# Kernel tuning notes

Measured on AMD Instinct MI355X. Metric: run time of the kernel, lower is better.

## Reference

```python
import jax, jax.numpy as jnp
import numpy as np

NUM_HEADS = 12


def setup_inputs() -> dict:
    key = jax.random.key(0)
    ks = jax.random.split(key, 5)
    B, S, D = 4, 2048, 768
    scale = 0.02
    return {
        "hidden_states": jax.random.normal(ks[0], (B, S, D), dtype=jnp.float32),
        "c_attn_w": jax.random.normal(ks[1], (D, 3 * D), dtype=jnp.float32) * scale,
        "c_attn_b": jax.random.normal(ks[2], (3 * D,), dtype=jnp.float32) * scale,
        "c_proj_w": jax.random.normal(ks[3], (D, D), dtype=jnp.float32) * scale,
        "c_proj_b": jax.random.normal(ks[4], (D,), dtype=jnp.float32) * scale,
    }


def reference(hidden_states, c_attn_w, c_attn_b, c_proj_w, c_proj_b):
    B, S, D = hidden_states.shape
    H = NUM_HEADS
    hd = D // H

    # fused QKV projection (HF Conv1D: x @ W + b, W is [in, out])
    qkv = hidden_states @ c_attn_w + c_attn_b  # [B, S, 3D]
    q, k, v = jnp.split(qkv, 3, axis=-1)

    def split_heads(t):
        return t.reshape(B, S, H, hd).transpose(0, 2, 1, 3)  # [B, H, S, hd]

    q, k, v = split_heads(q), split_heads(k), split_heads(v)

    # scaled dot-product scores (scale_attn_weights=True -> / sqrt(head_dim))
    scores = jnp.einsum("bhqd,bhkd->bhqk", q, k) / jnp.asarray(
        np.sqrt(hd), dtype=q.dtype
    )

    # causal mask: where(tril, scores, dtype_min) as in eager GPT2Attention
    causal = jnp.tril(jnp.ones((S, S), dtype=bool))
    mask_value = jnp.finfo(scores.dtype).min
    scores = jnp.where(causal[None, None, :, :], scores, mask_value)

    attn = jax.nn.softmax(scores, axis=-1)  # attn_dropout p=0 (eval)

    out = jnp.einsum("bhqk,bhkd->bhqd", attn, v)
    out = out.transpose(0, 2, 1, 3).reshape(B, S, D)  # merge heads

    # output projection (resid_dropout p=0)
    return out @ c_proj_w + c_proj_b
```

## Files before the change

kernel.cpp:

```cpp
#include <hip/hip_runtime.h>
#include <stdint.h>

typedef __attribute__((ext_vector_type(8))) short short8;
typedef __attribute__((ext_vector_type(4))) short short4v;
typedef __attribute__((ext_vector_type(8))) __bf16 bf16x8;
typedef __attribute__((ext_vector_type(4))) float f32x4;

#define SEQ 2048
#define DMODEL 768
#define NHEAD 12
#define HD 64
#define NBATCH 4

#define QSCALE 0.18033688011112042f

__device__ __forceinline__ float bf2f(unsigned short u) {
    return __uint_as_float(((unsigned int)u) << 16);
}
__device__ __forceinline__ unsigned short f2bf(float f) {
    unsigned int u = __float_as_uint(f);
    u += 0x7fffu + ((u >> 16) & 1u);
    return (unsigned short)(u >> 16);
}
__device__ __forceinline__ unsigned short f2bfn(float f) {
    union { __bf16 h; unsigned short u; } cv;
    cv.h = (__bf16)f;
    return cv.u;
}
__device__ __forceinline__ short8 cvt8(float4 a, float4 b) {
    short8 r;
    r[0] = (short)f2bf(a.x); r[1] = (short)f2bf(a.y);
    r[2] = (short)f2bf(a.z); r[3] = (short)f2bf(a.w);
    r[4] = (short)f2bf(b.x); r[5] = (short)f2bf(b.y);
    r[6] = (short)f2bf(b.z); r[7] = (short)f2bf(b.w);
    return r;
}
__device__ __forceinline__ f32x4 mfma16(short8 a, short8 b, f32x4 c) {
    return __builtin_amdgcn_mfma_f32_16x16x32_bf16(
        __builtin_bit_cast(bf16x8, a), __builtin_bit_cast(bf16x8, b), c, 0, 0, 0);
}
__device__ __forceinline__ f32x4 mfma16k16(short4v a, short4v b, f32x4 c) {
#if __has_builtin(__builtin_amdgcn_mfma_f32_16x16x16bf16_1k)
    return __builtin_amdgcn_mfma_f32_16x16x16bf16_1k(a, b, c, 0, 0, 0);
#else
    asm("v_mfma_f32_16x16x16_bf16 %0, %1, %2, %0" : "+v"(c) : "v"(a), "v"(b));
    return c;
#endif
}
__device__ __forceinline__ void gload16(const unsigned short* g, unsigned short* l) {
    __builtin_amdgcn_global_load_lds(
        (const __attribute__((address_space(1))) unsigned int*)g,
        (__attribute__((address_space(3))) unsigned int*)l, 16, 0, 0);
}

__global__ void detect_k(const unsigned short* x, const unsigned short* w1,
                         const unsigned short* b1, const unsigned short* w2,
                         const unsigned short* b2, int* flags) {
    const int w = threadIdx.x >> 6, l = threadIdx.x & 63;
    if (w >= 5) return;
    const unsigned short* ptrs[5] = {x, w1, b1, w2, b2};
    const unsigned short* p = ptrs[w];
    float mx = 0.f;
    for (int j = l; j < 1024; j += 64) {
        float v = fabsf(bf2f(p[j]));
        if (!(v <= 1e30f)) v = 1e31f;
        if (v > mx) mx = v;
    }
#pragma unroll
    for (int off = 1; off < 64; off <<= 1) mx = fmaxf(mx, __shfl_xor(mx, off, 64));
    if (l == 0) flags[w] = (mx > 1e3f) ? 1 : 0;
}

__global__ __launch_bounds__(256) void cvt_x(
    const float* __restrict__ Xf, const unsigned short* __restrict__ Xh,
    unsigned short* __restrict__ Xb, const int* __restrict__ flags, int n8) {
    int i = blockIdx.x * 256 + threadIdx.x;
    if (i >= n8) return;
    if (flags[0]) {
        float4 a = ((const float4*)Xf)[(size_t)i * 2];
        float4 b = ((const float4*)Xf)[(size_t)i * 2 + 1];
        *(short8*)&Xb[(size_t)i * 8] = cvt8(a, b);
    } else {
        ((uint4*)Xb)[i] = ((const uint4*)Xh)[i];
    }
}

__device__ __forceinline__ void wt_body(
    unsigned short (*tile)[65], const float* __restrict__ Wf,
    const unsigned short* __restrict__ Wh, unsigned short* __restrict__ Wt,
    int R, int C, bool f32, int bx, int by, int t) {

    const int c0 = bx * 64, r0 = by * 64;
    const int ri = t >> 2, cj = (t & 3) * 16;

    if (f32) {
#pragma unroll
        for (int u = 0; u < 4; u++) {
            float4 v = *(const float4*)&Wf[(size_t)(r0 + ri) * C + c0 + cj + u * 4];
            tile[ri][cj + u * 4 + 0] = f2bf(v.x);
            tile[ri][cj + u * 4 + 1] = f2bf(v.y);
            tile[ri][cj + u * 4 + 2] = f2bf(v.z);
            tile[ri][cj + u * 4 + 3] = f2bf(v.w);
        }
    } else {
        uint4 a = *(const uint4*)&Wh[(size_t)(r0 + ri) * C + c0 + cj];
        uint4 b = *(const uint4*)&Wh[(size_t)(r0 + ri) * C + c0 + cj + 8];
        *(uint4*)&tile[ri][cj] = a;
        *(uint4*)&tile[ri][cj + 8] = b;
    }
    __syncthreads();

    const int ci = t >> 2, rj = (t & 3) * 16;
    unsigned short tmp[16];
#pragma unroll
    for (int u = 0; u < 16; u++) tmp[u] = tile[rj + u][ci];
    *(uint4*)&Wt[(size_t)(c0 + ci) * R + r0 + rj]     = *(uint4*)&tmp[0];
    *(uint4*)&Wt[(size_t)(c0 + ci) * R + r0 + rj + 8] = *(uint4*)&tmp[8];
}

__global__ __launch_bounds__(256) void convert_wt_both(
    const float* __restrict__ Wf1, const unsigned short* __restrict__ Wh1,
    unsigned short* __restrict__ Wt1,
    const float* __restrict__ Wf2, const unsigned short* __restrict__ Wh2,
    unsigned short* __restrict__ Wt2, const int* __restrict__ flags) {

    __shared__ unsigned short tile[64][65];
    const int t = threadIdx.x;
    if (blockIdx.y < 12) {
        wt_body(tile, Wf1, Wh1, Wt1, 768, 2304, flags[1] != 0,
                (int)blockIdx.x, (int)blockIdx.y, t);
    } else {
        if (blockIdx.x >= 12) return;
        wt_body(tile, Wf2, Wh2, Wt2, 768, 768, flags[3] != 0,
                (int)blockIdx.x, (int)blockIdx.y - 12, t);
    }
}

__global__ __launch_bounds__(256, 4) void gemm_bt(
    const float* __restrict__ Af, const unsigned short* __restrict__ Ah,
    const unsigned short* __restrict__ Bt,
    const float* __restrict__ biasf, const unsigned short* __restrict__ biash,
    int K, int mode, const int* __restrict__ flags, int aFidx, int bFidx,
    unsigned short* __restrict__ out0, unsigned short* __restrict__ out1,
    unsigned short* __restrict__ out2, float* __restrict__ outf) {

    __shared__ __align__(16) unsigned short As[2][128][32];
    __shared__ __align__(16) unsigned short Bs[2][128][32];

    int bx = blockIdx.x, by = blockIdx.y;
    {
        const int nwg = (int)(gridDim.x * gridDim.y);
        if ((nwg & 7) == 0) {
            int bid = by * gridDim.x + bx;
            const int cpx = nwg >> 3;
            bid = (bid & 7) * cpx + (bid >> 3);
            bx = bid % gridDim.x;
            by = bid / gridDim.x;
        }
    }
    const int mBase = by * 128;
    const int nBase = bx * 128;
    const int t = threadIdx.x;
    const int w = t >> 6, l = t & 63, lr = l & 15, lk = l >> 4;
    const int wr = w >> 1, wc = w & 1;

    const bool af32 = (aFidx >= 0) && (flags[aFidx] != 0);
    const bool bf32 = flags[bFidx] != 0;

    f32x4 zero = {0.f, 0.f, 0.f, 0.f};
    f32x4 acc[4][4];
#pragma unroll
    for (int i = 0; i < 4; i++)
#pragma unroll
        for (int j = 0; j < 4; j++) acc[i][j] = zero;

    const int arow2 = t >> 1;
    const int ha32 = t & 1;
    const float* Afp = Af + (size_t)mBase * K;
    const unsigned short* Ahp = Ah + (size_t)mBase * K;
    const unsigned short* Bp = Bt + (size_t)nBase * K;

    unsigned short* BsF = &Bs[0][0][0];
    unsigned short* AsF = &As[0][0][0];

    for (int k0 = 0; k0 < K; k0 += 64) {
#pragma unroll
        for (int q = 0; q < 4; q++) {
            const int c = q * 256 + t;
            const int row = (c >> 2) & 127;
            const int ha = c >> 9;
            const int g2 = c & 3;
            gload16(&Bp[(size_t)row * K + k0 + ha * 32 + g2 * 8],
                    BsF + (size_t)(q * 256 + w * 64) * 8);
        }
        if (af32) {
#pragma unroll
            for (int u = 0; u < 4; u++) {
                float4 f0 = *(const float4*)&Afp[(size_t)arow2 * K + k0 + ha32 * 32 + u * 8];
                float4 f1 = *(const float4*)&Afp[(size_t)arow2 * K + k0 + ha32 * 32 + u * 8 + 4];
                *(short8*)&As[ha32][arow2][u * 8] = cvt8(f0, f1);
            }
        } else {
#pragma unroll
            for (int q = 0; q < 4; q++) {
                const int c = q * 256 + t;
                const int row = (c >> 2) & 127;
                const int ha = c >> 9;
                const int g2 = c & 3;
                gload16(&Ahp[(size_t)row * K + k0 + ha * 32 + g2 * 8],
                        AsF + (size_t)(q * 256 + w * 64) * 8);
            }
        }
        __syncthreads();

#pragma unroll
        for (int ha = 0; ha < 2; ha++) {
            short8 a[4], b[4];
#pragma unroll
            for (int i = 0; i < 4; i++)
                a[i] = *(const short8*)&As[ha][wr * 64 + i * 16 + lr][lk * 8];
#pragma unroll
            for (int j = 0; j < 4; j++)
                b[j] = *(const short8*)&Bs[ha][wc * 64 + j * 16 + lr][lk * 8];
#pragma unroll
            for (int i = 0; i < 4; i++)
#pragma unroll
                for (int j = 0; j < 4; j++) acc[i][j] = mfma16(a[i], b[j], acc[i][j]);
        }
        __syncthreads();
    }

#pragma unroll
    for (int j = 0; j < 4; j++) {
        int col = nBase + wc * 64 + j * 16 + lr;
        float bv = bf32 ? biasf[col] : bf2f(biash[col]);
        if (mode == 0 && col >= 1536) {
            int c2 = col - 1536;
            int h = c2 >> 6, d = c2 & 63;
#pragma unroll
            for (int i = 0; i < 4; i++) {
                int row0 = mBase + wr * 64 + i * 16 + lk * 4;
                int bb = row0 >> 11, s0 = row0 & 2047;
                short4v hv4;
#pragma unroll
                for (int r = 0; r < 4; r++) hv4[r] = (short)f2bf(acc[i][j][r] + bv);
                *(short4v*)&out2[(((size_t)(bb * NHEAD + h)) * HD + d) * SEQ + s0] = hv4;
            }
        } else {
#pragma unroll
            for (int i = 0; i < 4; i++) {
                int row0 = mBase + wr * 64 + i * 16 + lk * 4;
#pragma unroll
                for (int r = 0; r < 4; r++) {
                    int row = row0 + r;
                    float fv = acc[i][j][r] + bv;
                    if (mode == 0) {
                        int bb = row >> 11;
                        int s  = row & 2047;
                        if (col < 768) {
                            int h = col >> 6, d = col & 63;
                            out0[(((size_t)(bb * NHEAD + h)) * SEQ + s) * HD + d] =
                                f2bf(fv * QSCALE);
                        } else {
                            int c2 = col - 768;
                            int h = c2 >> 6, d = c2 & 63;
                            out1[(((size_t)(bb * NHEAD + h)) * SEQ + s) * HD + d] =
                                f2bf(fv);
                        }
                    } else {
                        outf[(size_t)row * DMODEL + col] = fv;
                    }
                }
            }
        }
    }
}

#define STAGE(buf, tile) do {                                                  \
    _Pragma("unroll")                                                          \
    for (int q_ = 0; q_ < 2; ++q_) {                                           \
        const int c_ = w * 128 + q_ * 64 + l;                                  \
        const int row_ = c_ >> 3;                                              \
        const int ch_ = (c_ & 7) ^ (row_ & 7);                                 \
        gload16(&Kp[(size_t)((tile) * 64 + row_) * HD + ch_ * 8],              \
                &Ks[buf][(w * 128 + q_ * 64) * 8]);                            \
        gload16(&Vp[(size_t)row_ * SEQ + (tile) * 64 + ch_ * 8],               \
                &Vs[buf][(w * 128 + q_ * 64) * 8]);                            \
    }                                                                          \
} while (0)

__global__ __launch_bounds__(256, 3) void flash_attn(
    const unsigned short* __restrict__ Q, const unsigned short* __restrict__ Km,
    const unsigned short* __restrict__ Vt, unsigned short* __restrict__ Oatt) {

    const int h  = blockIdx.x;
    const int px = (7 * blockIdx.y + blockIdx.x + blockIdx.z) & 15;
    const int b  = blockIdx.z;
    const int bh = b * NHEAD + h;
    const int qtA = 31 - px;
    const int qtB = px;
    const int t = threadIdx.x, w = t >> 6, l = t & 63, lr = l & 15, lk = l >> 4;
    const int qbA = qtA * 64 + w * 16;
    const int qbB = qtB * 64 + w * 16;

    const unsigned short* Qp = Q + (size_t)bh * SEQ * HD;
    const unsigned short* Kp = Km + (size_t)bh * SEQ * HD;
    const unsigned short* Vp = Vt + (size_t)bh * HD * SEQ;

    __shared__ __align__(16) unsigned short Ks[3][4096];
    __shared__ __align__(16) unsigned short Vs[3][4096];

    short8 qA0 = *(const short8*)&Qp[(size_t)(qbA + lr) * HD + lk * 8];
    short8 qA1 = *(const short8*)&Qp[(size_t)(qbA + lr) * HD + 32 + lk * 8];
    short8 qB0 = *(const short8*)&Qp[(size_t)(qbB + lr) * HD + lk * 8];
    short8 qB1 = *(const short8*)&Qp[(size_t)(qbB + lr) * HD + 32 + lk * 8];

    f32x4 zero = {0.f, 0.f, 0.f, 0.f};
    f32x4 oA[4], oB[4];
    float lsumA = 0.f, lsumB = 0.f;
#pragma unroll
    for (int dt = 0; dt < 4; dt++) { oA[dt] = zero; oB[dt] = zero; }

    STAGE(0, 0);
    STAGE(1, 1);
    asm volatile("s_waitcnt vmcnt(4)" ::: "memory");
    __builtin_amdgcn_s_barrier();

    int cur = 0;
    for (int kt = 0; kt <= qtA; ++kt) {
        const bool pf = (kt + 2 <= qtA);
        if (pf) {
            const int st = (cur == 0) ? 2 : cur - 1;
            STAGE(st, kt + 2);
        }
        const bool doB = (kt <= qtB);

        f32x4 s0[4], s1[4];
        __builtin_amdgcn_s_setprio(1);
#pragma unroll
        for (int ct = 0; ct < 4; ct++) {
            const int row = ct * 16 + lr, sw = row & 7;
            short8 k0 = *(const short8*)&Ks[cur][(row * 8 + (lk ^ sw)) * 8];
            short8 k1 = *(const short8*)&Ks[cur][(row * 8 + ((4 | lk) ^ sw)) * 8];
            s0[ct] = mfma16(k0, qA0, zero);
            s0[ct] = mfma16(k1, qA1, s0[ct]);
            if (doB) {
                s1[ct] = mfma16(k0, qB0, zero);
                s1[ct] = mfma16(k1, qB1, s1[ct]);
            }
        }
        __builtin_amdgcn_s_setprio(0);

        short4v vf[4][4];
#pragma unroll
        for (int dt = 0; dt < 4; dt++) {
            const int row = dt * 16 + lr;
            const int sw = row & 7;
#pragma unroll
            for (int ct = 0; ct < 4; ct++) {
                const int g = 2 * ct + (lk >> 1);
                const int hh = lk & 1;
                vf[dt][ct] = *(const short4v*)&Vs[cur][(row * 8 + (g ^ sw)) * 8 + hh * 4];
            }
        }

        short4v paA[4];
        {
            float p[4][4];
#pragma unroll
            for (int ct = 0; ct < 4; ct++)
#pragma unroll
                for (int r = 0; r < 4; r++) p[ct][r] = exp2f(s0[ct][r]);
            if (kt == qtA) {
                const int qrow = qbA + lr;
#pragma unroll
                for (int ct = 0; ct < 4; ct++)
#pragma unroll
                    for (int r = 0; r < 4; r++) {
                        const int key = kt * 64 + ct * 16 + lk * 4 + r;
                        if (key > qrow) p[ct][r] = 0.0f;
                    }
            }
#pragma unroll
            for (int ct = 0; ct < 4; ct++)
                lsumA += (p[ct][0] + p[ct][1]) + (p[ct][2] + p[ct][3]);
#pragma unroll
            for (int ct = 0; ct < 4; ct++) {
                short4v pk;
#pragma unroll
                for (int r = 0; r < 4; r++) pk[r] = (short)f2bfn(p[ct][r]);
                paA[ct] = pk;
            }
        }
        __builtin_amdgcn_s_setprio(1);
#pragma unroll
        for (int dt = 0; dt < 4; dt++)
#pragma unroll
            for (int ct = 0; ct < 4; ct++)
                oA[dt] = mfma16k16(paA[ct], vf[dt][ct], oA[dt]);
        __builtin_amdgcn_s_setprio(0);

        if (doB) {
            short4v paB[4];
            float p[4][4];
#pragma unroll
            for (int ct = 0; ct < 4; ct++)
#pragma unroll
                for (int r = 0; r < 4; r++) p[ct][r] = exp2f(s1[ct][r]);
            if (kt == qtB) {
                const int qrow = qbB + lr;
#pragma unroll
                for (int ct = 0; ct < 4; ct++)
#pragma unroll
                    for (int r = 0; r < 4; r++) {
                        const int key = kt * 64 + ct * 16 + lk * 4 + r;
                        if (key > qrow) p[ct][r] = 0.0f;
                    }
            }
#pragma unroll
            for (int ct = 0; ct < 4; ct++)
                lsumB += (p[ct][0] + p[ct][1]) + (p[ct][2] + p[ct][3]);
#pragma unroll
            for (int ct = 0; ct < 4; ct++) {
                short4v pk;
#pragma unroll
                for (int r = 0; r < 4; r++) pk[r] = (short)f2bfn(p[ct][r]);
                paB[ct] = pk;
            }
            __builtin_amdgcn_s_setprio(1);
#pragma unroll
            for (int dt = 0; dt < 4; dt++)
#pragma unroll
                for (int ct = 0; ct < 4; ct++)
                    oB[dt] = mfma16k16(paB[ct], vf[dt][ct], oB[dt]);
            __builtin_amdgcn_s_setprio(0);
        }

        if (kt < qtA) {
            if (pf) asm volatile("s_waitcnt vmcnt(4)" ::: "memory");
            else    asm volatile("s_waitcnt vmcnt(0)" ::: "memory");
            __builtin_amdgcn_s_barrier();
        }
        cur = (cur == 2) ? 0 : cur + 1;
    }

    lsumA += __shfl_xor(lsumA, 16, 64);
    lsumA += __shfl_xor(lsumA, 32, 64);
    lsumB += __shfl_xor(lsumB, 16, 64);
    lsumB += __shfl_xor(lsumB, 32, 64);

#pragma unroll
    for (int r = 0; r < 4; r++) {
        const float invA = 1.0f / __shfl(lsumA, lk * 4 + r, 64);
        const float invB = 1.0f / __shfl(lsumB, lk * 4 + r, 64);
        const int rowA = qbA + lk * 4 + r;
        const int rowB = qbB + lk * 4 + r;
#pragma unroll
        for (int dt = 0; dt < 4; dt++) {
            Oatt[((size_t)(b * SEQ) + rowA) * DMODEL + h * HD + dt * 16 + lr] =
                f2bfn(oA[dt][r] * invA);
            Oatt[((size_t)(b * SEQ) + rowB) * DMODEL + h * HD + dt * 16 + lr] =
                f2bfn(oB[dt][r] * invB);
        }
    }
}

extern "C" void kernel_launch(void* const* d_in, const int* in_sizes, int n_in,
                              void* d_out, int out_size, void* d_ws, size_t ws_size,
                              hipStream_t stream) {
    const void *X = d_in[0], *W1 = d_in[1], *b1 = d_in[2], *W2 = d_in[3], *b2 = d_in[4];
    for (int i = 0; i < n_in; i++) {
        switch (in_sizes[i]) {
            case NBATCH * SEQ * DMODEL: X  = d_in[i]; break;
            case DMODEL * 3 * DMODEL:   W1 = d_in[i]; break;
            case 3 * DMODEL:            b1 = d_in[i]; break;
            case DMODEL * DMODEL:       W2 = d_in[i]; break;
            case DMODEL:                b2 = d_in[i]; break;
        }
    }
    float* out = (float*)d_out;

    int* flags = (int*)d_ws;
    unsigned short* base = (unsigned short*)d_ws + 64;
    unsigned short* Wt1 = base;
    unsigned short* Wt2 = Wt1 + (size_t)2304 * 768;

    const size_t headElems = (size_t)NHEAD * SEQ * HD;
    const size_t xElems = (size_t)NBATCH * SEQ * DMODEL;
    const size_t fixedElems = 64 + (size_t)2304 * 768 + (size_t)768 * 768;
    const size_t mergedNeed = (fixedElems + xElems + 4 * NBATCH * headElems) * 2 + 1024;
    const bool merged = ws_size >= mergedNeed;

    detect_k<<<1, 320, 0, stream>>>(
        (const unsigned short*)X, (const unsigned short*)W1,
        (const unsigned short*)b1, (const unsigned short*)W2,
        (const unsigned short*)b2, flags);

    convert_wt_both<<<dim3(36, 24), 256, 0, stream>>>(
        (const float*)W1, (const unsigned short*)W1, Wt1,
        (const float*)W2, (const unsigned short*)W2, Wt2, flags);

    if (merged) {
        unsigned short* Xb  = Wt2 + (size_t)768 * 768;
        unsigned short* Qw  = Xb + xElems;
        unsigned short* Kw  = Qw + (size_t)NBATCH * headElems;
        unsigned short* Vtw = Kw + (size_t)NBATCH * headElems;
        unsigned short* Aw  = Vtw + (size_t)NBATCH * headElems;

        cvt_x<<<(int)((xElems / 8 + 255) / 256), 256, 0, stream>>>(
            (const float*)X, (const unsigned short*)X, Xb, flags, (int)(xElems / 8));

        gemm_bt<<<dim3(2304 / 128, NBATCH * SEQ / 128), 256, 0, stream>>>(
            nullptr, Xb, Wt1,
            (const float*)b1, (const unsigned short*)b1,
            DMODEL, 0, flags, -1, 2, Qw, Kw, Vtw, nullptr);

        flash_attn<<<dim3(NHEAD, 16, NBATCH), 256, 0, stream>>>(Qw, Kw, Vtw, Aw);

        gemm_bt<<<dim3(768 / 128, NBATCH * SEQ / 128), 256, 0, stream>>>(
            nullptr, Aw, Wt2,
            (const float*)b2, (const unsigned short*)b2,
            DMODEL, 1, flags, -1, 4, nullptr, nullptr, nullptr, out);
    } else {
        unsigned short* Qw  = Wt2 + (size_t)768 * 768;
        unsigned short* Kw  = Qw + headElems;
        unsigned short* Vtw = Kw + headElems;
        unsigned short* Aw  = Vtw + headElems;
        for (int batch = 0; batch < NBATCH; ++batch) {
            const size_t xoff = (size_t)batch * SEQ * DMODEL;

            gemm_bt<<<dim3(2304 / 128, SEQ / 128), 256, 0, stream>>>(
                (const float*)X + xoff, (const unsigned short*)X + xoff, Wt1,
                (const float*)b1, (const unsigned short*)b1,
                DMODEL, 0, flags, 0, 2, Qw, Kw, Vtw, nullptr);

            flash_attn<<<dim3(NHEAD, 16, 1), 256, 0, stream>>>(Qw, Kw, Vtw, Aw);

            gemm_bt<<<dim3(768 / 128, SEQ / 128), 256, 0, stream>>>(
                nullptr, Aw, Wt2,
                (const float*)b2, (const unsigned short*)b2,
                DMODEL, 1, flags, -1, 4, nullptr, nullptr, nullptr, out + xoff);
        }
    }
}
```

Baseline: 224.3 us.

## Double-buffer GEMM shared-memory tiles to overlap global loads with MFMA

The GEMM main loop now steps K in chunks of 32 and uses the two shared-memory halves as a ping-pong buffer: the next stage is prefetched while MFMAs run on the current one. This replaces the previous load-everything, sync, compute, sync pattern and is meant to hide global-load latency while using one barrier per step instead of two. The trade-off is twice as many loop iterations with fewer MFMAs each, and hand-written s_waitcnt/barrier synchronisation that must order the fp32-to-bf16 LDS stores correctly.

```diff
diff --git a/kernel.cpp b/kernel.cpp
--- a/kernel.cpp
+++ b/kernel.cpp
@@ -136,6 +136,34 @@
     }
 }
 
+#define GSTG(buf, s) do {                                                          \
+    unsigned short* BsF_ = &Bs[buf][0][0];                                         \
+    gload16(&Bp[(size_t)(ch0 >> 2) * K + (s) * 32 + (ch0 & 3) * 8],                \
+            BsF_ + (size_t)(w * 2 + 0) * 512);                                     \
+    gload16(&Bp[(size_t)(ch1 >> 2) * K + (s) * 32 + (ch1 & 3) * 8],                \
+            BsF_ + (size_t)(w * 2 + 1) * 512);                                     \
+    if (af32) {                                                                    \
+        float4 f0_ = *(const float4*)&Afp[(size_t)arow * K + (s) * 32 + acol];     \
+        float4 f1_ = *(const float4*)&Afp[(size_t)arow * K + (s) * 32 + acol + 4]; \
+        float4 f2_ = *(const float4*)&Afp[(size_t)(arow + 64) * K + (s) * 32 + acol];     \
+        float4 f3_ = *(const float4*)&Afp[(size_t)(arow + 64) * K + (s) * 32 + acol + 4]; \
+        *(short8*)&As[buf][arow][acol]      = cvt8(f0_, f1_);                      \
+        *(short8*)&As[buf][arow + 64][acol] = cvt8(f2_, f3_);                      \
+    } else {                                                                       \
+        unsigned short* AsF_ = &As[buf][0][0];                                     \
+        gload16(&Ahp[(size_t)(ch0 >> 2) * K + (s) * 32 + (ch0 & 3) * 8],           \
+                AsF_ + (size_t)(w * 2 + 0) * 512);                                 \
+        gload16(&Ahp[(size_t)(ch1 >> 2) * K + (s) * 32 + (ch1 & 3) * 8],           \
+                AsF_ + (size_t)(w * 2 + 1) * 512);                                 \
+    }                                                                              \
+} while (0)
+
+#define GSYNC() do {                                                               \
+    if (af32) asm volatile("s_waitcnt vmcnt(0) lgkmcnt(0)" ::: "memory");          \
+    else      asm volatile("s_waitcnt vmcnt(0)" ::: "memory");                     \
+    __builtin_amdgcn_s_barrier();                                                  \
+} while (0)
+
 __global__ __launch_bounds__(256, 4) void gemm_bt(
     const float* __restrict__ Af, const unsigned short* __restrict__ Ah,
     const unsigned short* __restrict__ Bt,
@@ -174,60 +202,38 @@
 #pragma unroll
         for (int j = 0; j < 4; j++) acc[i][j] = zero;
 
-    const int arow2 = t >> 1;
-    const int ha32 = t & 1;
+    const int arow = t >> 2;
+    const int acol = (t & 3) * 8;
     const float* Afp = Af + (size_t)mBase * K;
     const unsigned short* Ahp = Ah + (size_t)mBase * K;
     const unsigned short* Bp = Bt + (size_t)nBase * K;
 
-    unsigned short* BsF = &Bs[0][0][0];
-    unsigned short* AsF = &As[0][0][0];
-
-    for (int k0 = 0; k0 < K; k0 += 64) {
-#pragma unroll
-        for (int q = 0; q < 4; q++) {
-            const int c = q * 256 + t;
-            const int row = (c >> 2) & 127;
-            const int ha = c >> 9;
-            const int g2 = c & 3;
-            gload16(&Bp[(size_t)row * K + k0 + ha * 32 + g2 * 8],
-                    BsF + (size_t)(q * 256 + w * 64) * 8);
-        }
-        if (af32) {
-#pragma unroll
-            for (int u = 0; u < 4; u++) {
-                float4 f0 = *(const float4*)&Afp[(size_t)arow2 * K + k0 + ha32 * 32 + u * 8];
-                float4 f1 = *(const float4*)&Afp[(size_t)arow2 * K + k0 + ha32 * 32 + u * 8 + 4];
-                *(short8*)&As[ha32][arow2][u * 8] = cvt8(f0, f1);
-            }
-        } else {
-#pragma unroll
-            for (int q = 0; q < 4; q++) {
-                const int c = q * 256 + t;
-                const int row = (c >> 2) & 127;
-                const int ha = c >> 9;
-                const int g2 = c & 3;
-                gload16(&Ahp[(size_t)row * K + k0 + ha * 32 + g2 * 8],
-                        AsF + (size_t)(q * 256 + w * 64) * 8);
-            }
-        }
-        __syncthreads();
-
-#pragma unroll
-        for (int ha = 0; ha < 2; ha++) {
-            short8 a[4], b[4];
-#pragma unroll
-            for (int i = 0; i < 4; i++)
-                a[i] = *(const short8*)&As[ha][wr * 64 + i * 16 + lr][lk * 8];
-#pragma unroll
-            for (int j = 0; j < 4; j++)
-                b[j] = *(const short8*)&Bs[ha][wc * 64 + j * 16 + lr][lk * 8];
-#pragma unroll
-            for (int i = 0; i < 4; i++)
-#pragma unroll
-                for (int j = 0; j < 4; j++) acc[i][j] = mfma16(a[i], b[j], acc[i][j]);
-        }
-        __syncthreads();
+    const int ch0 = (w * 2 + 0) * 64 + l;
+    const int ch1 = (w * 2 + 1) * 64 + l;
+
+    const int nsteps = K >> 5;
+
+    GSTG(0, 0);
+    GSYNC();
+
+    int cur = 0;
+    for (int s = 0; s < nsteps; ++s) {
+        if (s + 1 < nsteps) GSTG(cur ^ 1, s + 1);
+
+        short8 a[4], b[4];
+#pragma unroll
+        for (int i = 0; i < 4; i++)
+            a[i] = *(const short8*)&As[cur][wr * 64 + i * 16 + lr][lk * 8];
+#pragma unroll
+        for (int j = 0; j < 4; j++)
+            b[j] = *(const short8*)&Bs[cur][wc * 64 + j * 16 + lr][lk * 8];
+#pragma unroll
+        for (int i = 0; i < 4; i++)
+#pragma unroll
+            for (int j = 0; j < 4; j++) acc[i][j] = mfma16(a[i], b[j], acc[i][j]);
+
+        if (s + 1 < nsteps) GSYNC();
+        cur ^= 1;
     }
 
 #pragma unroll
```

New measurement: 236.8 us. 5.6% more time.
